# Performance work log

Measured on AMD Instinct MI355X. Metric: run time of the kernel, lower is better.

The kernel has to match this reference:

```python
import jax, jax.numpy as jnp
import numpy as np

B, T, D, H, OUT = 16384, 25, 128, 128, 128


def setup_inputs() -> dict:
    key = jax.random.key(0)
    ks = jax.random.split(key, 7)
    s = lambda k, shape, fan: jax.random.normal(k, shape, jnp.float32) / np.sqrt(fan)
    return {
        "self_vecs": jax.random.normal(ks[0], (B, D), jnp.float32),
        "neig_vecs": jax.random.normal(ks[1], (B, T, D), jnp.float32),
        "kernel": s(ks[2], (D, 4 * H), D),          # LSTM input kernel (gate order i,f,g,o)
        "rec_kernel": s(ks[3], (H, 4 * H), H),      # LSTM recurrent kernel
        "lstm_bias": jnp.zeros((4 * H,), jnp.float32).at[H:2 * H].set(1.0),  # unit forget bias
        "W_self": s(ks[4], (D, OUT), D),
        "W_neigh": s(ks[5], (H, OUT), H),
    }


def _lstm_seq(x, kernel, rec_kernel, bias):
    # x: [B, T, D] -> all hidden states [B, T, H]
    xW = jnp.einsum("btd,dg->btg", x, kernel) + bias  # [B, T, 4H]
    h0 = jnp.zeros((x.shape[0], rec_kernel.shape[0]), x.dtype)
    c0 = jnp.zeros_like(h0)

    def step(carry, xt):
        h, c = carry
        z = xt + h @ rec_kernel  # [B, 4H]
        i, f, g, o = jnp.split(z, 4, axis=-1)
        i = jax.nn.sigmoid(i)
        f = jax.nn.sigmoid(f)
        g = jnp.tanh(g)
        o = jax.nn.sigmoid(o)
        c = f * c + i * g
        h = o * jnp.tanh(c)
        return (h, c), h

    _, hs = jax.lax.scan(step, (h0, c0), jnp.swapaxes(xW, 0, 1))  # hs: [T, B, H]
    return jnp.swapaxes(hs, 0, 1)


def reference(self_vecs, neig_vecs, kernel, rec_kernel, lstm_bias, W_self, W_neigh):
    # sequence lengths from non-zero neighbor rows (min 1)
    used = jnp.sign(jnp.max(jnp.abs(neig_vecs), axis=2))          # [B, T]
    length = jnp.maximum(jnp.sum(used, axis=1), 1.0).astype(jnp.int32)  # [B]
    hs = _lstm_seq(neig_vecs, kernel, rec_kernel, lstm_bias)      # [B, T, H]
    neigh_h = jnp.take_along_axis(hs, (length - 1)[:, None, None], axis=1)[:, 0, :]  # [B, H]
    out = self_vecs @ W_self + neigh_h @ W_neigh
    return jax.nn.relu(out)
```

## Files before the change

### kernel.cpp

```cpp
#include <hip/hip_runtime.h>
#include <hip/hip_bf16.h>
#include <stdint.h>


typedef __attribute__((ext_vector_type(8))) short bf16x8;
typedef __attribute__((ext_vector_type(4))) float f32x4;

#define MFMA16(a, b, c) __builtin_amdgcn_mfma_f32_16x16x32_bf16(a, b, c, 0, 0, 0)

#define NB      16384
#define TSEQ    25
#define DIM     128
#define G4      512
#define ROWSTRB (TSEQ * DIM * 4)

#define WC_OFF    0
#define WOUT_OFF  (256 * 1024)
#define LEN_OFF   (256 * 1024 + 64 * 1024)

__device__ __forceinline__ unsigned short bf16_bits(float f) {
  unsigned u = __builtin_bit_cast(unsigned, f);
  u += 0x7FFFu + ((u >> 16) & 1u);
  return (unsigned short)(u >> 16);
}

__device__ __forceinline__ unsigned pk2(float lo, float hi) {
  return (unsigned)bf16_bits(lo) | ((unsigned)bf16_bits(hi) << 16);
}

__device__ __forceinline__ bf16x8 cvt8(f32x4 a, f32x4 b) {
  union { bf16x8 v; unsigned u[4]; } r;
  r.u[0] = pk2(a[0], a[1]);
  r.u[1] = pk2(a[2], a[3]);
  r.u[2] = pk2(b[0], b[1]);
  r.u[3] = pk2(b[2], b[3]);
  return r.v;
}

__device__ __forceinline__ void gload_lds16(const void* g, void* l) {
  __builtin_amdgcn_global_load_lds(
      (const __attribute__((address_space(1))) unsigned int*)g,
      (__attribute__((address_space(3))) unsigned int*)l, 16, 0, 0);
}

#define L2E 1.4426950408889634f
__device__ __forceinline__ float sigm(float x) {
  return __builtin_amdgcn_rcpf(1.0f + __builtin_amdgcn_exp2f(-L2E * x));
}
__device__ __forceinline__ float tanh_(float x) {
  return 2.0f * __builtin_amdgcn_rcpf(1.0f + __builtin_amdgcn_exp2f(-2.0f * L2E * x)) - 1.0f;
}

__global__ void k_pack(const float* __restrict__ kern, const float* __restrict__ rec,
                       const float* __restrict__ wself, const float* __restrict__ wneigh,
                       unsigned char* __restrict__ ws) {
  int tid = blockIdx.x * 256 + threadIdx.x;
  if (tid < 16384) {
    int frag = tid >> 6, lane = tid & 63;
    int w = frag >> 5, j = (frag >> 3) & 3, kk = frag & 7;
    int col = (w + 8 * j) * 16 + (lane & 15);
    int k0 = kk * 32 + (lane >> 4) * 8;
    unsigned u[4];
    #pragma unroll
    for (int p = 0; p < 4; ++p) {
      int ka = k0 + 2 * p, kb = ka + 1;
      float va = (ka < 128) ? kern[ka * G4 + col] : rec[(ka - 128) * G4 + col];
      float vb = (kb < 128) ? kern[kb * G4 + col] : rec[(kb - 128) * G4 + col];
      u[p] = (unsigned)bf16_bits(va) | ((unsigned)bf16_bits(vb) << 16);
    }
    uint4 o = make_uint4(u[0], u[1], u[2], u[3]);
    *(uint4*)(ws + WC_OFF + (size_t)frag * 1024 + lane * 16) = o;
  } else if (tid < 16384 + 4096) {
    int t2 = tid - 16384;
    int frag = t2 >> 6, lane = t2 & 63;
    int w = frag >> 3, kk = frag & 7;
    int col = w * 16 + (lane & 15);
    int k0 = kk * 32 + (lane >> 4) * 8;
    unsigned u[4];
    #pragma unroll
    for (int p = 0; p < 4; ++p) {
      int ka = k0 + 2 * p, kb = ka + 1;
      float va = (ka < 128) ? wself[ka * DIM + col] : wneigh[(ka - 128) * DIM + col];
      float vb = (kb < 128) ? wself[kb * DIM + col] : wneigh[(kb - 128) * DIM + col];
      u[p] = (unsigned)bf16_bits(va) | ((unsigned)bf16_bits(vb) << 16);
    }
    uint4 o = make_uint4(u[0], u[1], u[2], u[3]);
    *(uint4*)(ws + WOUT_OFF + (size_t)frag * 1024 + lane * 16) = o;
  }
}

__global__ void k_len(const float* __restrict__ neig, int* __restrict__ len) {
  int wid = (blockIdx.x * 256 + threadIdx.x) >> 6;
  int lane = threadIdx.x & 63;
  if (wid >= NB) return;
  const float* base = neig + (size_t)wid * TSEQ * DIM;
  int cnt = 0;
  for (int t = 0; t < TSEQ; ++t) {
    float2 v = *(const float2*)(base + t * DIM + lane * 2);
    cnt += (__any(v.x != 0.0f || v.y != 0.0f) ? 1 : 0);
  }
  if (lane == 0) len[wid] = cnt > 0 ? cnt : 1;
}

__launch_bounds__(512, 2)
__global__ void k_main(const float* __restrict__ self, const float* __restrict__ neig,
                       const float* __restrict__ bias, const unsigned char* __restrict__ ws,
                       float* __restrict__ out) {
  __shared__ alignas(16) unsigned char smem[81920];
  const int tid  = threadIdx.x;
  const int lane = tid & 63;
  const int w    = tid >> 6;
  const int qh   = lane >> 4;
  const int ql   = lane & 15;
  const int b0   = blockIdx.x * 64;

  bf16x8 bw[4][8];
  {
    const unsigned char* base = ws + WC_OFF + (size_t)(w * 32) * 1024 + lane * 16;
    #pragma unroll
    for (int j = 0; j < 4; ++j)
      #pragma unroll
      for (int kk = 0; kk < 8; ++kk)
        bw[j][kk] = *(const bf16x8*)(base + (j * 8 + kk) * 1024);
  }
  float bgate[4];
  #pragma unroll
  for (int j = 0; j < 4; ++j) bgate[j] = bias[j * 128 + w * 16 + ql];
  const int* lenp = (const int*)(ws + LEN_OFF);
  unsigned lp[4];
  #pragma unroll
  for (int m = 0; m < 4; ++m) {
    unsigned v = 0;
    #pragma unroll
    for (int r = 0; r < 4; ++r)
      v |= ((unsigned)lenp[b0 + 16 * m + qh * 4 + r]) << (8 * r);
    lp[m] = v;
  }
  f32x4 c[4];
  #pragma unroll
  for (int m = 0; m < 4; ++m) c[m] = (f32x4){0.f, 0.f, 0.f, 0.f};
  unsigned hcap[4][2] = {{0u,0u},{0u,0u},{0u,0u},{0u,0u}};

  *(uint4*)(smem + 65536 + tid * 32)      = make_uint4(0, 0, 0, 0);
  *(uint4*)(smem + 65536 + tid * 32 + 16) = make_uint4(0, 0, 0, 0);

  unsigned voff[4];
  #pragma unroll
  for (int i = 0; i < 4; ++i) {
    int row = 8 * w + 2 * i + (lane >> 5);
    int ch  = (lane & 31) ^ (row & 7);
    voff[i] = (unsigned)(row * ROWSTRB + ch * 16);
  }
  const unsigned char* gneig = (const unsigned char*)neig + (size_t)b0 * ROWSTRB;

  #pragma unroll
  for (int i = 0; i < 4; ++i)
    gload_lds16(gneig + voff[i], smem + (8 * w + 2 * i) * 512);
  asm volatile("s_waitcnt vmcnt(0)" ::: "memory");
  __syncthreads();

  int cur = 0;
  for (int t = 0; t < TSEQ; ++t) {
    {
      int tn = (t < TSEQ - 1) ? t + 1 : TSEQ - 1;
      const unsigned char* g = gneig + tn * 512;
      unsigned lb = (unsigned)((cur ^ 1) * 32768);
      #pragma unroll
      for (int i = 0; i < 4; ++i)
        gload_lds16(g + voff[i], smem + lb + (8 * w + 2 * i) * 512);
    }
    f32x4 acc[4][4];
    #pragma unroll
    for (int m = 0; m < 4; ++m)
      #pragma unroll
      for (int j = 0; j < 4; ++j) acc[m][j] = (f32x4){0.f, 0.f, 0.f, 0.f};
    {
      const unsigned xb = (unsigned)(cur * 32768);
      #pragma unroll
      for (int m = 0; m < 4; ++m) {
        const int row = 16 * m + ql;
        const int rs  = row & 7;
        #pragma unroll
        for (int kk = 0; kk < 4; ++kk) {
          int c0 = kk * 8 + qh * 2;
          f32x4 v0 = *(const f32x4*)(smem + xb + row * 512 + ((c0)     ^ rs) * 16);
          f32x4 v1 = *(const f32x4*)(smem + xb + row * 512 + ((c0 + 1) ^ rs) * 16);
          bf16x8 a = cvt8(v0, v1);
          #pragma unroll
          for (int j = 0; j < 4; ++j)
            acc[m][j] = MFMA16(a, bw[j][kk], acc[m][j]);
        }
        #pragma unroll
        for (int kk = 0; kk < 4; ++kk) {
          bf16x8 a = *(const bf16x8*)(smem + 65536 + row * 256 + ((kk * 4 + qh) ^ rs) * 16);
          #pragma unroll
          for (int j = 0; j < 4; ++j)
            acc[m][j] = MFMA16(a, bw[j][kk + 4], acc[m][j]);
        }
      }
    }
    __syncthreads();
    const unsigned tp1 = (unsigned)(t + 1);
    #pragma unroll
    for (int m = 0; m < 4; ++m) {
      float hh[4];
      #pragma unroll
      for (int r = 0; r < 4; ++r) {
        float ii = sigm(acc[m][0][r] + bgate[0]);
        float ff = sigm(acc[m][1][r] + bgate[1]);
        float gg = tanh_(acc[m][2][r] + bgate[2]);
        float oo = sigm(acc[m][3][r] + bgate[3]);
        float cc = ff * c[m][r] + ii * gg;
        c[m][r] = cc;
        hh[r] = oo * tanh_(cc);
      }
      #pragma unroll
      for (int r = 0; r < 4; ++r) {
        int row = 16 * m + qh * 4 + r;
        unsigned addr = 65536u + row * 256 + (((2 * w + (ql >> 3)) ^ (row & 7)) * 16) + (ql & 7) * 2;
        *(unsigned short*)(smem + addr) = bf16_bits(hh[r]);
      }
      #pragma unroll
      for (int p = 0; p < 2; ++p) {
        unsigned pk = pk2(hh[2 * p], hh[2 * p + 1]);
        unsigned m0 = (((lp[m] >> (16 * p))     & 255u) == tp1) ? 0x0000FFFFu : 0u;
        unsigned m1 = (((lp[m] >> (16 * p + 8)) & 255u) == tp1) ? 0xFFFF0000u : 0u;
        unsigned msk = m0 | m1;
        hcap[m][p] = (msk & pk) | (~msk & hcap[m][p]);
      }
    }
    asm volatile("s_waitcnt vmcnt(0)" ::: "memory");
    __syncthreads();
    cur ^= 1;
  }

  {
    int row = tid >> 3, seg = tid & 7;
    const float* src = self + (size_t)(b0 + row) * DIM + seg * 16;
    float4 f0 = *(const float4*)(src);
    float4 f1 = *(const float4*)(src + 4);
    float4 f2 = *(const float4*)(src + 8);
    float4 f3 = *(const float4*)(src + 12);
    uint4 o0 = make_uint4(pk2(f0.x, f0.y), pk2(f0.z, f0.w), pk2(f1.x, f1.y), pk2(f1.z, f1.w));
    uint4 o1 = make_uint4(pk2(f2.x, f2.y), pk2(f2.z, f2.w), pk2(f3.x, f3.y), pk2(f3.z, f3.w));
    int rs = row & 7;
    *(uint4*)(smem + row * 256 + ((seg * 2)     ^ rs) * 16) = o0;
    *(uint4*)(smem + row * 256 + ((seg * 2 + 1) ^ rs) * 16) = o1;
  }
  #pragma unroll
  for (int m = 0; m < 4; ++m)
    #pragma unroll
    for (int p = 0; p < 2; ++p)
      #pragma unroll
      for (int hi2 = 0; hi2 < 2; ++hi2) {
        int r = 2 * p + hi2;
        int row = 16 * m + qh * 4 + r;
        unsigned addr = 65536u + row * 256 + (((2 * w + (ql >> 3)) ^ (row & 7)) * 16) + (ql & 7) * 2;
        *(unsigned short*)(smem + addr) = (unsigned short)((hcap[m][p] >> (16 * hi2)) & 0xFFFFu);
      }
  __syncthreads();
  bf16x8 bo[8];
  #pragma unroll
  for (int kk = 0; kk < 8; ++kk)
    bo[kk] = *(const bf16x8*)(ws + WOUT_OFF + (size_t)(w * 8 + kk) * 1024 + lane * 16);
  #pragma unroll
  for (int m = 0; m < 4; ++m) {
    const int row = 16 * m + ql;
    const int rs  = row & 7;
    f32x4 a2 = (f32x4){0.f, 0.f, 0.f, 0.f};
    #pragma unroll
    for (int kk = 0; kk < 4; ++kk) {
      bf16x8 a = *(const bf16x8*)(smem + row * 256 + ((kk * 4 + qh) ^ rs) * 16);
      a2 = MFMA16(a, bo[kk], a2);
    }
    #pragma unroll
    for (int kk = 0; kk < 4; ++kk) {
      bf16x8 a = *(const bf16x8*)(smem + 65536 + row * 256 + ((kk * 4 + qh) ^ rs) * 16);
      a2 = MFMA16(a, bo[kk + 4], a2);
    }
    #pragma unroll
    for (int r = 0; r < 4; ++r) {
      float v = a2[r] > 0.0f ? a2[r] : 0.0f;
      out[(size_t)(b0 + 16 * m + qh * 4 + r) * DIM + w * 16 + ql] = v;
    }
  }
}

extern "C" void kernel_launch(void* const* d_in, const int* in_sizes, int n_in,
                              void* d_out, int out_size, void* d_ws, size_t ws_size,
                              hipStream_t stream) {
  const float* self   = (const float*)d_in[0];
  const float* neig   = (const float*)d_in[1];
  const float* kern   = (const float*)d_in[2];
  const float* rec    = (const float*)d_in[3];
  const float* lbias  = (const float*)d_in[4];
  const float* wself  = (const float*)d_in[5];
  const float* wneigh = (const float*)d_in[6];
  float* out = (float*)d_out;
  unsigned char* ws = (unsigned char*)d_ws;

  k_pack<<<80, 256, 0, stream>>>(kern, rec, wself, wneigh, ws);
  k_len<<<4096, 256, 0, stream>>>(neig, (int*)(ws + LEN_OFF));
  k_main<<<256, 512, 0, stream>>>(self, neig, lbias, ws, out);
}
```

Measured before the change: 776.2 us.

## Precompute input projection for all timesteps before the LSTM recurrence kernel

Splits the fused LSTM kernel into three. A fully parallel MFMA GEMM computes x·W + bias for every (batch, timestep) into a large bf16 workspace buffer and records which neighbor rows are non-zero. A small kernel turns those flags into sequence lengths. The recurrent kernel then only does h·U (K=128 instead of 256) per step and streams the precomputed gate inputs into LDS with double buffering. This takes half the matrix work off the serial critical path, at the cost of writing and re-reading about 400 MB of intermediate data, written with scattered 2-byte stores. The new path runs only when the workspace is large enough; otherwise it falls back to the old kernels.

```diff
diff --git a/kernel.cpp b/kernel.cpp
--- a/kernel.cpp
+++ b/kernel.cpp
@@ -16,18 +16,19 @@
 
 #define WC_OFF    0
 #define WOUT_OFF  (256 * 1024)
-#define LEN_OFF   (256 * 1024 + 64 * 1024)
+#define LEN_OFF   (320 * 1024)
+#define USED_OFF  (384 * 1024)
+#define XZ_OFF    819200
+#define WS_NEED   (819200ull + 419430400ull)
 
 __device__ __forceinline__ unsigned short bf16_bits(float f) {
   unsigned u = __builtin_bit_cast(unsigned, f);
   u += 0x7FFFu + ((u >> 16) & 1u);
   return (unsigned short)(u >> 16);
 }
-
 __device__ __forceinline__ unsigned pk2(float lo, float hi) {
   return (unsigned)bf16_bits(lo) | ((unsigned)bf16_bits(hi) << 16);
 }
-
 __device__ __forceinline__ bf16x8 cvt8(f32x4 a, f32x4 b) {
   union { bf16x8 v; unsigned u[4]; } r;
   r.u[0] = pk2(a[0], a[1]);
@@ -36,13 +37,11 @@
   r.u[3] = pk2(b[2], b[3]);
   return r.v;
 }
-
 __device__ __forceinline__ void gload_lds16(const void* g, void* l) {
   __builtin_amdgcn_global_load_lds(
       (const __attribute__((address_space(1))) unsigned int*)g,
       (__attribute__((address_space(3))) unsigned int*)l, 16, 0, 0);
 }
-
 #define L2E 1.4426950408889634f
 __device__ __forceinline__ float sigm(float x) {
   return __builtin_amdgcn_rcpf(1.0f + __builtin_amdgcn_exp2f(-L2E * x));
@@ -68,8 +67,7 @@
       float vb = (kb < 128) ? kern[kb * G4 + col] : rec[(kb - 128) * G4 + col];
       u[p] = (unsigned)bf16_bits(va) | ((unsigned)bf16_bits(vb) << 16);
     }
-    uint4 o = make_uint4(u[0], u[1], u[2], u[3]);
-    *(uint4*)(ws + WC_OFF + (size_t)frag * 1024 + lane * 16) = o;
+    *(uint4*)(ws + WC_OFF + (size_t)frag * 1024 + lane * 16) = make_uint4(u[0], u[1], u[2], u[3]);
   } else if (tid < 16384 + 4096) {
     int t2 = tid - 16384;
     int frag = t2 >> 6, lane = t2 & 63;
@@ -84,8 +82,254 @@
       float vb = (kb < 128) ? wself[kb * DIM + col] : wneigh[(kb - 128) * DIM + col];
       u[p] = (unsigned)bf16_bits(va) | ((unsigned)bf16_bits(vb) << 16);
     }
-    uint4 o = make_uint4(u[0], u[1], u[2], u[3]);
-    *(uint4*)(ws + WOUT_OFF + (size_t)frag * 1024 + lane * 16) = o;
+    *(uint4*)(ws + WOUT_OFF + (size_t)frag * 1024 + lane * 16) = make_uint4(u[0], u[1], u[2], u[3]);
+  }
+}
+
+__launch_bounds__(256, 3)
+__global__ void k1_xw(const float* __restrict__ neig, const float* __restrict__ bias,
+                      const unsigned char* __restrict__ ws,
+                      unsigned char* __restrict__ used, unsigned char* __restrict__ xz) {
+  const int gw = (blockIdx.x * 256 + threadIdx.x) >> 6;
+  const int nw = (gridDim.x * 256) >> 6;
+  const int lane = threadIdx.x & 63, qh = lane >> 4, ql = lane & 15;
+
+  for (int tile = gw; tile < 25600; tile += nw) {
+    const int r0 = tile * 16;
+    const float* xbase = neig + (size_t)r0 * 128;
+    bf16x8 a[4];
+    unsigned orr = 0;
+    #pragma unroll
+    for (int kk = 0; kk < 4; ++kk) {
+      f32x4 v0 = *(const f32x4*)(xbase + ql * 128 + kk * 32 + qh * 8);
+      f32x4 v1 = *(const f32x4*)(xbase + ql * 128 + kk * 32 + qh * 8 + 4);
+      #pragma unroll
+      for (int e = 0; e < 4; ++e)
+        orr |= __float_as_uint(v0[e]) | __float_as_uint(v1[e]);
+      a[kk] = cvt8(v0, v1);
+    }
+    orr |= __shfl_xor(orr, 16);
+    orr |= __shfl_xor(orr, 32);
+    if (lane < 16) used[r0 + ql] = ((orr << 1) != 0u) ? 1 : 0;
+    size_t zb[4]; unsigned sw[4];
+    #pragma unroll
+    for (int r = 0; r < 4; ++r) {
+      unsigned R = (unsigned)(r0 + qh * 4 + r);
+      unsigned b = (unsigned)(((unsigned long long)R * 0x51EB851Full) >> 35);
+      unsigned t = R - b * 25;
+      zb[r] = ((size_t)t * NB + b) * 1024;
+      sw[r] = (b & 7) << 4;
+    }
+    #pragma unroll 1
+    for (int nn = 0; nn < 8; ++nn) {
+      bf16x8 bwf[4][4];
+      #pragma unroll
+      for (int nl = 0; nl < 4; ++nl) {
+        int ng = nn * 4 + nl;
+        const unsigned char* fb = ws + WC_OFF + (size_t)((ng & 7) * 32 + (ng >> 3) * 8) * 1024 + lane * 16;
+        #pragma unroll
+        for (int kk = 0; kk < 4; ++kk)
+          bwf[nl][kk] = *(const bf16x8*)(fb + kk * 1024);
+      }
+      f32x4 acc[4];
+      #pragma unroll
+      for (int nl = 0; nl < 4; ++nl) acc[nl] = (f32x4){0.f, 0.f, 0.f, 0.f};
+      #pragma unroll
+      for (int kk = 0; kk < 4; ++kk)
+        #pragma unroll
+        for (int nl = 0; nl < 4; ++nl)
+          acc[nl] = MFMA16(a[kk], bwf[nl][kk], acc[nl]);
+      #pragma unroll
+      for (int nl = 0; nl < 4; ++nl) {
+        int ng = nn * 4 + nl;
+        int col = ng * 16 + ql;
+        float bs = bias[col];
+        #pragma unroll
+        for (int r = 0; r < 4; ++r) {
+          float v = acc[nl][r] + bs;
+          *(unsigned short*)(xz + zb[r] + (((unsigned)col * 2) ^ sw[r])) = bf16_bits(v);
+        }
+      }
+    }
+  }
+}
+
+__global__ void k_len2(const unsigned char* __restrict__ used, int* __restrict__ len) {
+  int b = blockIdx.x * 256 + threadIdx.x;
+  if (b >= NB) return;
+  const unsigned char* u = used + (size_t)b * 25;
+  int cnt = 0;
+  #pragma unroll
+  for (int t = 0; t < 25; ++t) cnt += u[t];
+  len[b] = cnt ? cnt : 1;
+}
+
+#define HOFF 131072u
+__launch_bounds__(512, 2)
+__global__ void k2_recur(const float* __restrict__ self, const unsigned char* __restrict__ ws,
+                         float* __restrict__ out) {
+  __shared__ alignas(16) unsigned char smem[147456];
+  const int tid  = threadIdx.x;
+  const int lane = tid & 63;
+  const int w    = tid >> 6;
+  const int qh   = lane >> 4;
+  const int ql   = lane & 15;
+  const int b0   = blockIdx.x * 64;
+
+  bf16x8 bw[4][4];
+  {
+    const unsigned char* base = ws + WC_OFF + (size_t)(w * 32 + 4) * 1024 + lane * 16;
+    #pragma unroll
+    for (int j = 0; j < 4; ++j)
+      #pragma unroll
+      for (int kk = 0; kk < 4; ++kk)
+        bw[j][kk] = *(const bf16x8*)(base + (j * 8 + kk) * 1024);
+  }
+  const int* lenp = (const int*)(ws + LEN_OFF);
+  unsigned lp[4];
+  #pragma unroll
+  for (int m = 0; m < 4; ++m) {
+    unsigned v = 0;
+    #pragma unroll
+    for (int r = 0; r < 4; ++r)
+      v |= ((unsigned)lenp[b0 + 16 * m + qh * 4 + r]) << (8 * r);
+    lp[m] = v;
+  }
+  f32x4 c[4];
+  #pragma unroll
+  for (int m = 0; m < 4; ++m) c[m] = (f32x4){0.f, 0.f, 0.f, 0.f};
+  unsigned hcap[4][2] = {{0u,0u},{0u,0u},{0u,0u},{0u,0u}};
+
+  *(uint4*)(smem + HOFF + tid * 32)      = make_uint4(0, 0, 0, 0);
+  *(uint4*)(smem + HOFF + tid * 32 + 16) = make_uint4(0, 0, 0, 0);
+
+  const unsigned char* gxz = ws + XZ_OFF;
+  {
+    const unsigned char* g = gxz + ((size_t)0 * NB + b0) * 1024;
+    #pragma unroll
+    for (int i = 0; i < 8; ++i)
+      gload_lds16(g + (8 * w + i) * 1024 + lane * 16, smem + (8 * w + i) * 1024);
+  }
+  asm volatile("s_waitcnt vmcnt(0)" ::: "memory");
+  __syncthreads();
+
+  int cur = 0;
+  for (int t = 0; t < TSEQ; ++t) {
+    {
+      int tn = (t < TSEQ - 1) ? t + 1 : TSEQ - 1;
+      const unsigned char* g = gxz + ((size_t)tn * NB + b0) * 1024;
+      unsigned lb = (unsigned)((cur ^ 1) * 65536);
+      #pragma unroll
+      for (int i = 0; i < 8; ++i)
+        gload_lds16(g + (8 * w + i) * 1024 + lane * 16, smem + lb + (8 * w + i) * 1024);
+    }
+    f32x4 acc[4][4];
+    #pragma unroll
+    for (int m = 0; m < 4; ++m)
+      #pragma unroll
+      for (int j = 0; j < 4; ++j) acc[m][j] = (f32x4){0.f, 0.f, 0.f, 0.f};
+    #pragma unroll
+    for (int m = 0; m < 4; ++m) {
+      const int row = 16 * m + ql;
+      const int rs  = row & 7;
+      #pragma unroll
+      for (int kk = 0; kk < 4; ++kk) {
+        bf16x8 a = *(const bf16x8*)(smem + HOFF + row * 256 + ((kk * 4 + qh) ^ rs) * 16);
+        #pragma unroll
+        for (int j = 0; j < 4; ++j)
+          acc[m][j] = MFMA16(a, bw[j][kk], acc[m][j]);
+      }
+    }
+    __syncthreads();
+    const unsigned tp1 = (unsigned)(t + 1);
+    const unsigned zbuf = (unsigned)(cur * 65536);
+    #pragma unroll
+    for (int m = 0; m < 4; ++m) {
+      float hh[4];
+      #pragma unroll
+      for (int r = 0; r < 4; ++r) {
+        const int row = 16 * m + qh * 4 + r;
+        const unsigned zrow = zbuf + row * 1024;
+        const unsigned swz  = (unsigned)((row & 7) << 4);
+        const unsigned cb   = (unsigned)((w * 16 + ql) * 2);
+        float zi = __uint_as_float(((unsigned)*(const unsigned short*)(smem + zrow + ((cb +   0u) ^ swz))) << 16) + acc[m][0][r];
+        float zf = __uint_as_float(((unsigned)*(const unsigned short*)(smem + zrow + ((cb + 256u) ^ swz))) << 16) + acc[m][1][r];
+        float zg = __uint_as_float(((unsigned)*(const unsigned short*)(smem + zrow + ((cb + 512u) ^ swz))) << 16) + acc[m][2][r];
+        float zo = __uint_as_float(((unsigned)*(const unsigned short*)(smem + zrow + ((cb + 768u) ^ swz))) << 16) + acc[m][3][r];
+        float ii = sigm(zi), ff = sigm(zf), gg = tanh_(zg), oo = sigm(zo);
+        float cc = ff * c[m][r] + ii * gg;
+        c[m][r] = cc;
+        hh[r] = oo * tanh_(cc);
+      }
+      #pragma unroll
+      for (int r = 0; r < 4; ++r) {
+        int row = 16 * m + qh * 4 + r;
+        unsigned addr = HOFF + row * 256 + (((2 * w + (ql >> 3)) ^ (row & 7)) * 16) + (ql & 7) * 2;
+        *(unsigned short*)(smem + addr) = bf16_bits(hh[r]);
+      }
+      #pragma unroll
+      for (int p = 0; p < 2; ++p) {
+        unsigned pk = pk2(hh[2 * p], hh[2 * p + 1]);
+        unsigned m0 = (((lp[m] >> (16 * p))     & 255u) == tp1) ? 0x0000FFFFu : 0u;
+        unsigned m1 = (((lp[m] >> (16 * p + 8)) & 255u) == tp1) ? 0xFFFF0000u : 0u;
+        unsigned msk = m0 | m1;
+        hcap[m][p] = (msk & pk) | (~msk & hcap[m][p]);
+      }
+    }
+    asm volatile("s_waitcnt vmcnt(0)" ::: "memory");
+    __syncthreads();
+    cur ^= 1;
+  }
+
+  {
+    int row = tid >> 3, seg = tid & 7;
+    const float* src = self + (size_t)(b0 + row) * DIM + seg * 16;
+    float4 f0 = *(const float4*)(src);
+    float4 f1 = *(const float4*)(src + 4);
+    float4 f2 = *(const float4*)(src + 8);
+    float4 f3 = *(const float4*)(src + 12);
+    uint4 o0 = make_uint4(pk2(f0.x, f0.y), pk2(f0.z, f0.w), pk2(f1.x, f1.y), pk2(f1.z, f1.w));
+    uint4 o1 = make_uint4(pk2(f2.x, f2.y), pk2(f2.z, f2.w), pk2(f3.x, f3.y), pk2(f3.z, f3.w));
+    int rs = row & 7;
+    *(uint4*)(smem + row * 256 + ((seg * 2)     ^ rs) * 16) = o0;
+    *(uint4*)(smem + row * 256 + ((seg * 2 + 1) ^ rs) * 16) = o1;
+  }
+  #pragma unroll
+  for (int m = 0; m < 4; ++m)
+    #pragma unroll
+    for (int p = 0; p < 2; ++p)
+      #pragma unroll
+      for (int hi2 = 0; hi2 < 2; ++hi2) {
+        int r = 2 * p + hi2;
+        int row = 16 * m + qh * 4 + r;
+        unsigned addr = HOFF + row * 256 + (((2 * w + (ql >> 3)) ^ (row & 7)) * 16) + (ql & 7) * 2;
+        *(unsigned short*)(smem + addr) = (unsigned short)((hcap[m][p] >> (16 * hi2)) & 0xFFFFu);
+      }
+  __syncthreads();
+  bf16x8 bo[8];
+  #pragma unroll
+  for (int kk = 0; kk < 8; ++kk)
+    bo[kk] = *(const bf16x8*)(ws + WOUT_OFF + (size_t)(w * 8 + kk) * 1024 + lane * 16);
+  #pragma unroll
+  for (int m = 0; m < 4; ++m) {
+    const int row = 16 * m + ql;
+    const int rs  = row & 7;
+    f32x4 a2 = (f32x4){0.f, 0.f, 0.f, 0.f};
+    #pragma unroll
+    for (int kk = 0; kk < 4; ++kk) {
+      bf16x8 a = *(const bf16x8*)(smem + row * 256 + ((kk * 4 + qh) ^ rs) * 16);
+      a2 = MFMA16(a, bo[kk], a2);
+    }
+    #pragma unroll
+    for (int kk = 0; kk < 4; ++kk) {
+      bf16x8 a = *(const bf16x8*)(smem + HOFF + row * 256 + ((kk * 4 + qh) ^ rs) * 16);
+      a2 = MFMA16(a, bo[kk + 4], a2);
+    }
+    #pragma unroll
+    for (int r = 0; r < 4; ++r) {
+      float v = a2[r] > 0.0f ? a2[r] : 0.0f;
+      out[(size_t)(b0 + 16 * m + qh * 4 + r) * DIM + w * 16 + ql] = v;
+    }
   }
 }
 
@@ -113,7 +357,6 @@
   const int qh   = lane >> 4;
   const int ql   = lane & 15;
   const int b0   = blockIdx.x * 64;
-
   bf16x8 bw[4][8];
   {
     const unsigned char* base = ws + WC_OFF + (size_t)(w * 32) * 1024 + lane * 16;
@@ -140,10 +383,8 @@
   #pragma unroll
   for (int m = 0; m < 4; ++m) c[m] = (f32x4){0.f, 0.f, 0.f, 0.f};
   unsigned hcap[4][2] = {{0u,0u},{0u,0u},{0u,0u},{0u,0u}};
-
   *(uint4*)(smem + 65536 + tid * 32)      = make_uint4(0, 0, 0, 0);
   *(uint4*)(smem + 65536 + tid * 32 + 16) = make_uint4(0, 0, 0, 0);
-
   unsigned voff[4];
   #pragma unroll
   for (int i = 0; i < 4; ++i) {
@@ -152,13 +393,11 @@
     voff[i] = (unsigned)(row * ROWSTRB + ch * 16);
   }
   const unsigned char* gneig = (const unsigned char*)neig + (size_t)b0 * ROWSTRB;
-
   #pragma unroll
   for (int i = 0; i < 4; ++i)
     gload_lds16(gneig + voff[i], smem + (8 * w + 2 * i) * 512);
   asm volatile("s_waitcnt vmcnt(0)" ::: "memory");
   __syncthreads();
-
   int cur = 0;
   for (int t = 0; t < TSEQ; ++t) {
     {
@@ -233,7 +472,6 @@
     __syncthreads();
     cur ^= 1;
   }
-
   {
     int row = tid >> 3, seg = tid & 7;
     const float* src = self + (size_t)(b0 + row) * DIM + seg * 16;
@@ -300,6 +538,12 @@
   unsigned char* ws = (unsigned char*)d_ws;
 
   k_pack<<<80, 256, 0, stream>>>(kern, rec, wself, wneigh, ws);
-  k_len<<<4096, 256, 0, stream>>>(neig, (int*)(ws + LEN_OFF));
-  k_main<<<256, 512, 0, stream>>>(self, neig, lbias, ws, out);
-}
+  if (ws_size >= WS_NEED) {
+    k1_xw<<<1024, 256, 0, stream>>>(neig, lbias, ws, ws + USED_OFF, ws + XZ_OFF);
+    k_len2<<<64, 256, 0, stream>>>(ws + USED_OFF, (int*)(ws + LEN_OFF));
+    k2_recur<<<256, 512, 0, stream>>>(self, ws, out);
+  } else {
+    k_len<<<4096, 256, 0, stream>>>(neig, (int*)(ws + LEN_OFF));
+    k_main<<<256, 512, 0, stream>>>(self, neig, lbias, ws, out);
+  }
+}
```

Result: slower. 805.0 us (+3.7%).
